# Kernel optimization log

Measured on AMD Instinct MI355X. Metric: run time of the kernel, lower is better.

The kernel has to match this reference:

```python
import jax, jax.numpy as jnp
import numpy as np

B, D, N, H = 1024, 512, 16, 512  # batch, latent, branches, hidden


def _lrelu(v):
    return jnp.where(v >= 0, v, 0.1 * v)  # LeakyReLU(0.1)


def setup_inputs() -> dict:
    key = jax.random.key(0)
    ks = jax.random.split(key, 9)
    s = 0.02
    return {
        "x": jax.random.normal(ks[0], (B, D, N), dtype=jnp.float32),
        "Ws1": jax.random.normal(ks[1], (D, D), dtype=jnp.float32) * s,
        "bs1": jnp.zeros((D,), dtype=jnp.float32),
        "Ws2": jax.random.normal(ks[2], (D, D), dtype=jnp.float32) * s,
        "bs2": jnp.zeros((D,), dtype=jnp.float32),
        # per-branch binary classifiers: Linear(D,H)+LeakyReLU+Linear(H,1)
        "Wc1": jax.random.normal(ks[3], (N, D, H), dtype=jnp.float32) * s,
        "bc1": jnp.zeros((N, H), dtype=jnp.float32),
        "Wc2": jax.random.normal(ks[4], (N, H), dtype=jnp.float32) * s,
        "bc2": jnp.zeros((N,), dtype=jnp.float32),
    }


def reference(x, Ws1, bs1, Ws2, bs2, Wc1, bc1, Wc2, bc2):
    # x: [B, D, N] -> per-branch tokens [B, N, D]
    xb = jnp.transpose(x, (0, 2, 1))
    # shared MLP applied to every branch slice (same weights)
    h = _lrelu(xb @ Ws1 + bs1)
    shared = _lrelu(h @ Ws2 + bs2)  # [B, N, D]
    # per-branch classifier on its own branch slice -> sigmoid probs
    h1 = _lrelu(jnp.einsum('bnd,ndh->bnh', shared, Wc1) + bc1)
    logits = jnp.einsum('bnh,nh->bn', h1, Wc2) + bc2  # [B, N]
    out = jax.nn.sigmoid(logits)[:, None, :]  # [B, 1, N]
    # full pass: concat branch slices along batch (branch-major), every
    # classifier applied to the full stack -> raw logits
    full_in = jnp.transpose(shared, (1, 0, 2)).reshape(N * B, D)  # [M, D]
    h2 = _lrelu(jnp.einsum('md,ndh->mnh', full_in, Wc1) + bc1)  # [M, N, H]
    full_logits = jnp.einsum('mnh,nh->mn', h2, Wc2) + bc2  # [M, N]
    full_out = full_logits[:, None, :]  # [N*B, 1, N]
    return (out, full_out)
```

## Files before the change

kernel.cpp:

```cpp
#include <hip/hip_runtime.h>
#include <hip/hip_bf16.h>
#include <stdint.h>

#define Bq 1024
#define Dq 512
#define Nq 16
#define Hq 512
#define Mq (Bq*Nq)

typedef short v8s  __attribute__((ext_vector_type(8)));
typedef float v16f __attribute__((ext_vector_type(16)));

typedef __attribute__((address_space(3))) unsigned int as3_u32;
typedef __attribute__((address_space(1))) const unsigned int as1_u32;

__device__ __forceinline__ unsigned short f2bf(float f) {
  union { float f; unsigned u; } v; v.f = f;
  return (unsigned short)((v.u + 0x7fffu + ((v.u >> 16) & 1u)) >> 16);
}

__global__ void k_transpose_x(const float* __restrict__ x, unsigned short* __restrict__ xb) {
  __shared__ float lds[Dq][Nq + 1];
  const int b = blockIdx.x;
  const float* xi = x + (size_t)b * Dq * Nq;
  const int t = threadIdx.x;
  for (int p = 0; p < (Dq*Nq)/256; ++p) {
    int i = t + p*256;
    lds[i >> 4][i & (Nq-1)] = xi[i];
  }
  __syncthreads();
  unsigned short* o = xb + (size_t)b * Nq * Dq;
  for (int p = 0; p < (Dq*Nq)/256; ++p) {
    int i = t + p*256;
    o[i] = f2bf(lds[i & (Dq-1)][i >> 9]);
  }
}

__global__ void k_transpose_w(const float* __restrict__ Ws1, const float* __restrict__ Ws2,
                              const float* __restrict__ Wc1,
                              unsigned short* __restrict__ Ws1t, unsigned short* __restrict__ Ws2t,
                              unsigned short* __restrict__ Wc1t) {
  __shared__ float tile[32][33];
  const int z = blockIdx.z;
  const float* in;
  unsigned short* out;
  if (z == 0)      { in = Ws1; out = Ws1t; }
  else if (z == 1) { in = Ws2; out = Ws2t; }
  else             { in = Wc1 + (size_t)(z-2) * 512 * 512; out = Wc1t + (size_t)(z-2) * 512 * 512; }
  const int tx = threadIdx.x, ty = threadIdx.y;
  const int c0 = blockIdx.x * 32, r0 = blockIdx.y * 32;
#pragma unroll
  for (int j = 0; j < 4; ++j)
    tile[ty + j*8][tx] = in[(size_t)(r0 + ty + j*8) * 512 + c0 + tx];
  __syncthreads();
#pragma unroll
  for (int j = 0; j < 4; ++j) {
    int c = c0 + ty + j*8;
    int r = r0 + tx;
    out[(size_t)c * 512 + r] = f2bf(tile[tx][ty + j*8]);
  }
}

template<int MODE, int BM>
__global__ __launch_bounds__(256, 2)
void k_gemm(const unsigned short* __restrict__ A,
            const unsigned short* __restrict__ Bt,
            const float* __restrict__ bias,
            void* __restrict__ out_,
            const float* __restrict__ w2,
            int permute) {
  constexpr int BN = 128, BK = 32, KD = 512;
  constexpr int NI = (BM == 256) ? 4 : 2;
  constexpr int AG = BM / 16;
  constexpr int TG = AG + BN / 16;
  __shared__ __align__(16) unsigned short As[2][BM][BK];
  __shared__ __align__(16) unsigned short Bs[2][BN][BK];

  const int t = threadIdx.x;
  const int wave = t >> 6, lane = t & 63;
  const int wr = (BM == 256) ? wave : (wave >> 1);
  const int wc = (BM == 256) ? 0    : (wave & 1);
  const int l32 = lane & 31, kh0 = lane >> 5;
  const int bm = blockIdx.x * BM, bn = blockIdx.y * BN;
  const int z = blockIdx.z;

  const unsigned short* Bz = Bt + (size_t)z * KD * 512;
  const float* biasz = bias + (size_t)z * 512;

  const int lrow = lane >> 2;
  const int lslot = lane & 3;

  auto stage = [&](int buf, int kt) {
#pragma unroll
    for (int i = wave; i < TG; i += 4) {
      const int isA = (i < AG);
      const int r0 = (isA ? i : i - AG) * 16;
      const int row = r0 + lrow;
      const int cg = lslot ^ ((row >> 1) & 3);
      const unsigned short* g = isA ? &A [(size_t)(bm + row) * KD + kt*BK + cg*8]
                                    : &Bz[(size_t)(bn + row) * KD + kt*BK + cg*8];
      as3_u32* d = isA ? (as3_u32*)&As[buf][r0][0] : (as3_u32*)&Bs[buf][r0][0];
      __builtin_amdgcn_global_load_lds((as1_u32*)g, d, 16, 0, 0);
    }
  };

  v16f acc[2][NI] = {};

  stage(0, 0);
  __syncthreads();

  for (int kt = 0; kt < KD / BK; ++kt) {
    const int cur = kt & 1;
    if (kt + 1 < KD / BK) stage(cur ^ 1, kt + 1);

    v8s af[2][2], bf[NI][2];
#pragma unroll
    for (int mi = 0; mi < 2; ++mi) {
      int ra = wr*64 + mi*32 + l32;
#pragma unroll
      for (int kh = 0; kh < 2; ++kh) {
        int c = kh*2 + kh0;
        af[mi][kh] = *(const v8s*)&As[cur][ra][(c ^ ((ra >> 1) & 3)) * 8];
      }
    }
#pragma unroll
    for (int ni = 0; ni < NI; ++ni) {
      int rb = wc*64 + ni*32 + l32;
#pragma unroll
      for (int kh = 0; kh < 2; ++kh) {
        int c = kh*2 + kh0;
        bf[ni][kh] = *(const v8s*)&Bs[cur][rb][(c ^ ((rb >> 1) & 3)) * 8];
      }
    }
#pragma unroll
    for (int kh = 0; kh < 2; ++kh)
#pragma unroll
      for (int mi = 0; mi < 2; ++mi)
#pragma unroll
        for (int ni = 0; ni < NI; ++ni)
          acc[mi][ni] = __builtin_amdgcn_mfma_f32_32x32x16_bf16(af[mi][kh], bf[ni][kh], acc[mi][ni], 0, 0, 0);
    __syncthreads();
  }

  if (MODE == 0) {
    unsigned short* O = (unsigned short*)out_;
#pragma unroll
    for (int mi = 0; mi < 2; ++mi) {
#pragma unroll
      for (int ni = 0; ni < NI; ++ni) {
        int col = bn + wc*64 + ni*32 + l32;
        float bcol = biasz[col];
#pragma unroll
        for (int reg = 0; reg < 16; ++reg) {
          int rl = (reg & 3) + 8*(reg >> 2) + 4*kh0;
          int grow = bm + wr*64 + mi*32 + rl;
          int orow = permute ? ((grow & 15) * Bq + (grow >> 4)) : grow;
          float v = acc[mi][ni][reg] + bcol;
          v = v >= 0.f ? v : 0.1f * v;
          O[(size_t)orow * 512 + col] = f2bf(v);
        }
      }
    }
  } else {
    float* FL = (float*)out_;
    const float* w2z = w2 + (size_t)z * 512;
#pragma unroll
    for (int mi = 0; mi < 2; ++mi) {
#pragma unroll
      for (int reg = 0; reg < 16; ++reg) {
        int rl = (reg & 3) + 8*(reg >> 2) + 4*kh0;
        float s = 0.f;
#pragma unroll
        for (int ni = 0; ni < NI; ++ni) {
          int col = bn + ni*32 + l32;
          float v = acc[mi][ni][reg] + biasz[col];
          v = v >= 0.f ? v : 0.1f * v;
          s += v * w2z[col];
        }
#pragma unroll
        for (int off = 1; off < 32; off <<= 1)
          s += __shfl_xor(s, off, 64);
        if (l32 == 0) {
          int grow = bm + wave*64 + mi*32 + rl;
          atomicAdd(&FL[(size_t)grow * Nq + z], s);
        }
      }
    }
  }
}

__global__ void k_final(const float* __restrict__ fl, const float* __restrict__ bc2,
                        float* __restrict__ out) {
  int i = blockIdx.x * 256 + threadIdx.x;
  int m = i >> 4, n = i & 15;
  float v = fl[i] + bc2[n];
  out[Mq + i] = v;
  if (n == (m >> 10)) {
    int b = m & (Bq - 1);
    out[b * Nq + n] = 1.f / (1.f + __expf(-v));
  }
}

extern "C" void kernel_launch(void* const* d_in, const int* in_sizes, int n_in,
                              void* d_out, int out_size, void* d_ws, size_t ws_size,
                              hipStream_t stream) {
  (void)in_sizes; (void)n_in; (void)out_size; (void)ws_size;
  const float* x   = (const float*)d_in[0];
  const float* Ws1 = (const float*)d_in[1];
  const float* bs1 = (const float*)d_in[2];
  const float* Ws2 = (const float*)d_in[3];
  const float* bs2 = (const float*)d_in[4];
  const float* Wc1 = (const float*)d_in[5];
  const float* bc1 = (const float*)d_in[6];
  const float* Wc2 = (const float*)d_in[7];
  const float* bc2 = (const float*)d_in[8];

  char* ws = (char*)d_ws;
  unsigned short* Xb   = (unsigned short*)(ws);
  unsigned short* Hbuf = (unsigned short*)(ws + (size_t)16*1024*1024);
  unsigned short* Sm   = (unsigned short*)(ws + (size_t)32*1024*1024);
  unsigned short* Ws1t = (unsigned short*)(ws + (size_t)48*1024*1024);
  unsigned short* Ws2t = (unsigned short*)(ws + (size_t)48*1024*1024 + 512*1024);
  unsigned short* Wc1t = (unsigned short*)(ws + (size_t)49*1024*1024);
  float*          FL   = (float*)         (ws + (size_t)57*1024*1024);

  hipMemsetAsync(FL, 0, (size_t)Mq * Nq * sizeof(float), stream);

  k_transpose_x<<<Bq, 256, 0, stream>>>(x, Xb);
  k_transpose_w<<<dim3(16,16,18), dim3(32,8), 0, stream>>>(Ws1, Ws2, Wc1, Ws1t, Ws2t, Wc1t);

  k_gemm<0,128><<<dim3(128,4,1), 256, 0, stream>>>(Xb,   Ws1t, bs1, Hbuf, nullptr, 0);
  k_gemm<0,128><<<dim3(128,4,1), 256, 0, stream>>>(Hbuf, Ws2t, bs2, Sm,   nullptr, 1);
  k_gemm<1,256><<<dim3(64,4,16), 256, 0, stream>>>(Sm, Wc1t, bc1, FL, Wc2, 0);

  k_final<<<(Mq*Nq)/256, 256, 0, stream>>>(FL, bc2, (float*)d_out);
}
```

Baseline: 326.6 us.

## Restructure classifier GEMM to keep B fragments in registers, stage only A in LDS

New measurement: 432.2 us. 32.3% more time.

```diff
diff --git a/kernel.cpp b/kernel.cpp
--- a/kernel.cpp
+++ b/kernel.cpp
@@ -70,7 +70,7 @@
             const float* __restrict__ w2,
             int permute) {
   constexpr int BN = 128, BK = 32, KD = 512;
-  constexpr int NI = (BM == 256) ? 4 : 2;
+  constexpr int NI = 2;
   constexpr int AG = BM / 16;
   constexpr int TG = AG + BN / 16;
   __shared__ __align__(16) unsigned short As[2][BM][BK];
@@ -78,8 +78,7 @@
 
   const int t = threadIdx.x;
   const int wave = t >> 6, lane = t & 63;
-  const int wr = (BM == 256) ? wave : (wave >> 1);
-  const int wc = (BM == 256) ? 0    : (wave & 1);
+  const int wr = wave >> 1, wc = wave & 1;
   const int l32 = lane & 31, kh0 = lane >> 5;
   const int bm = blockIdx.x * BM, bn = blockIdx.y * BN;
   const int z = blockIdx.z;
@@ -142,48 +141,126 @@
     __syncthreads();
   }
 
-  if (MODE == 0) {
-    unsigned short* O = (unsigned short*)out_;
-#pragma unroll
-    for (int mi = 0; mi < 2; ++mi) {
-#pragma unroll
-      for (int ni = 0; ni < NI; ++ni) {
-        int col = bn + wc*64 + ni*32 + l32;
-        float bcol = biasz[col];
-#pragma unroll
-        for (int reg = 0; reg < 16; ++reg) {
-          int rl = (reg & 3) + 8*(reg >> 2) + 4*kh0;
-          int grow = bm + wr*64 + mi*32 + rl;
-          int orow = permute ? ((grow & 15) * Bq + (grow >> 4)) : grow;
-          float v = acc[mi][ni][reg] + bcol;
-          v = v >= 0.f ? v : 0.1f * v;
-          O[(size_t)orow * 512 + col] = f2bf(v);
-        }
-      }
-    }
-  } else {
-    float* FL = (float*)out_;
-    const float* w2z = w2 + (size_t)z * 512;
-#pragma unroll
-    for (int mi = 0; mi < 2; ++mi) {
+  unsigned short* O = (unsigned short*)out_;
+#pragma unroll
+  for (int mi = 0; mi < 2; ++mi) {
+#pragma unroll
+    for (int ni = 0; ni < NI; ++ni) {
+      int col = bn + wc*64 + ni*32 + l32;
+      float bcol = biasz[col];
 #pragma unroll
       for (int reg = 0; reg < 16; ++reg) {
         int rl = (reg & 3) + 8*(reg >> 2) + 4*kh0;
-        float s = 0.f;
-#pragma unroll
-        for (int ni = 0; ni < NI; ++ni) {
-          int col = bn + ni*32 + l32;
-          float v = acc[mi][ni][reg] + biasz[col];
-          v = v >= 0.f ? v : 0.1f * v;
-          s += v * w2z[col];
-        }
-#pragma unroll
-        for (int off = 1; off < 32; off <<= 1)
-          s += __shfl_xor(s, off, 64);
-        if (l32 == 0) {
-          int grow = bm + wave*64 + mi*32 + rl;
-          atomicAdd(&FL[(size_t)grow * Nq + z], s);
-        }
+        int grow = bm + wr*64 + mi*32 + rl;
+        int orow = permute ? ((grow & 15) * Bq + (grow >> 4)) : grow;
+        float v = acc[mi][ni][reg] + bcol;
+        v = v >= 0.f ? v : 0.1f * v;
+        O[(size_t)orow * 512 + col] = f2bf(v);
+      }
+    }
+  }
+}
+
+__global__ __launch_bounds__(256, 2)
+void k_gemm3(const unsigned short* __restrict__ A,
+             const unsigned short* __restrict__ Bt,
+             const float* __restrict__ bias,
+             float* __restrict__ FL,
+             const float* __restrict__ w2) {
+  constexpr int BM = 128, BK = 32, KD = 512, NKT = KD / BK;
+  __shared__ __align__(16) unsigned short As[BM][BK];
+
+  const int t = threadIdx.x;
+  const int wave = t >> 6, lane = t & 63;
+  const int wrm = wave >> 1, wrn = wave & 1;
+  const int l32 = lane & 31, kh0 = lane >> 5;
+  const int bm = blockIdx.x * BM;
+  const int bn = blockIdx.y * 256;
+  const int z = blockIdx.z;
+
+  const unsigned short* Bz = Bt + (size_t)z * KD * 512;
+  const float* biasz = bias + (size_t)z * 512;
+  const float* w2z = w2 + (size_t)z * 512;
+
+  const int lrow = lane >> 2;
+  const int lslot = lane & 3;
+
+  auto stageA = [&](int kt) {
+#pragma unroll
+    for (int p = 0; p < 2; ++p) {
+      const int r0 = (wave * 2 + p) * 16;
+      const int row = r0 + lrow;
+      const int cg = lslot ^ ((row >> 1) & 3);
+      __builtin_amdgcn_global_load_lds((as1_u32*)&A[(size_t)(bm + row) * KD + kt*BK + cg*8],
+                                       (as3_u32*)&As[r0][0], 16, 0, 0);
+    }
+  };
+
+  auto loadB = [&](int kt, v8s bf[4][2]) {
+#pragma unroll
+    for (int ni = 0; ni < 4; ++ni) {
+      const size_t rb = (size_t)(bn + wrn*128 + ni*32 + l32) * KD + kt*BK;
+#pragma unroll
+      for (int kh = 0; kh < 2; ++kh)
+        bf[ni][kh] = *(const v8s*)&Bz[rb + (kh*2 + kh0)*8];
+    }
+  };
+
+  v16f acc[2][4] = {};
+  v8s bfc[4][2], bfn[4][2];
+
+  loadB(0, bfc);
+  stageA(0);
+
+  auto body = [&](int kt, v8s bcur[4][2], v8s bnxt[4][2]) {
+    __syncthreads();
+    v8s af[2][2];
+#pragma unroll
+    for (int mi = 0; mi < 2; ++mi) {
+      int ra = wrm*64 + mi*32 + l32;
+#pragma unroll
+      for (int kh = 0; kh < 2; ++kh) {
+        int c = kh*2 + kh0;
+        af[mi][kh] = *(const v8s*)&As[ra][(c ^ ((ra >> 1) & 3)) * 8];
+      }
+    }
+    if (kt + 1 < NKT) loadB(kt + 1, bnxt);
+#pragma unroll
+    for (int kh = 0; kh < 2; ++kh)
+#pragma unroll
+      for (int mi = 0; mi < 2; ++mi)
+#pragma unroll
+        for (int ni = 0; ni < 4; ++ni)
+          acc[mi][ni] = __builtin_amdgcn_mfma_f32_32x32x16_bf16(af[mi][kh], bcur[ni][kh], acc[mi][ni], 0, 0, 0);
+    __syncthreads();
+    if (kt + 1 < NKT) stageA(kt + 1);
+  };
+
+#pragma unroll 1
+  for (int kt = 0; kt < NKT; kt += 2) {
+    body(kt, bfc, bfn);
+    body(kt + 1, bfn, bfc);
+  }
+
+#pragma unroll
+  for (int mi = 0; mi < 2; ++mi) {
+#pragma unroll
+    for (int reg = 0; reg < 16; ++reg) {
+      int rl = (reg & 3) + 8*(reg >> 2) + 4*kh0;
+      float s = 0.f;
+#pragma unroll
+      for (int ni = 0; ni < 4; ++ni) {
+        int col = bn + wrn*128 + ni*32 + l32;
+        float v = acc[mi][ni][reg] + biasz[col];
+        v = v >= 0.f ? v : 0.1f * v;
+        s += v * w2z[col];
+      }
+#pragma unroll
+      for (int off = 1; off < 32; off <<= 1)
+        s += __shfl_xor(s, off, 64);
+      if (l32 == 0) {
+        int grow = bm + wrm*64 + mi*32 + rl;
+        atomicAdd(&FL[(size_t)grow * Nq + z], s);
       }
     }
   }
@@ -231,7 +308,7 @@
 
   k_gemm<0,128><<<dim3(128,4,1), 256, 0, stream>>>(Xb,   Ws1t, bs1, Hbuf, nullptr, 0);
   k_gemm<0,128><<<dim3(128,4,1), 256, 0, stream>>>(Hbuf, Ws2t, bs2, Sm,   nullptr, 1);
-  k_gemm<1,256><<<dim3(64,4,16), 256, 0, stream>>>(Sm, Wc1t, bc1, FL, Wc2, 0);
+  k_gemm3<<<dim3(128,2,16), 256, 0, stream>>>(Sm, Wc1t, bc1, FL, Wc2);
 
   k_final<<<(Mq*Nq)/256, 256, 0, stream>>>(FL, bc2, (float*)d_out);
 }
```
